# Optimization experiments

Hardware: AMD Instinct MI355X
Metric: run time of the kernel (lower is better)

Reference implementation:

```python
import jax, jax.numpy as jnp
import numpy as np

NUM_HEADS = 10
LN_EPS = 1e-5


def setup_inputs() -> dict:
    key = jax.random.key(0)
    ks = jax.random.split(key, 6)
    N, D = 4096, 640  # in_dim == out_dim required by residual add
    x = jax.random.normal(ks[0], (N, D), dtype=jnp.float32)
    s = 1.0 / np.sqrt(D)
    Wq = jax.random.normal(ks[1], (D, D), dtype=jnp.float32) * s  # torch Linear weight [out,in]
    Wk = jax.random.normal(ks[2], (D, D), dtype=jnp.float32) * s
    Wv = jax.random.normal(ks[3], (D, D), dtype=jnp.float32) * s
    gamma = jnp.ones((D,), dtype=jnp.float32)
    beta = jnp.zeros((D,), dtype=jnp.float32)
    return {"x": x, "Wq": Wq, "Wk": Wk, "Wv": Wv, "gamma": gamma, "beta": beta}


def reference(x, Wq, Wk, Wv, gamma, beta):
    N, D = x.shape
    dk = D // NUM_HEADS
    Q = x @ Wq.T  # [N, D]
    K = x @ Wk.T
    V = x @ Wv.T
    # Faithful to source: raw reshapes (NOT transposes)
    Qh = Q.reshape(NUM_HEADS, N, dk)
    Kh = K.reshape(NUM_HEADS, N, dk).reshape(NUM_HEADS, dk, N)  # torch.reshape, not .mT
    Vh = V.reshape(NUM_HEADS, N, dk)
    # Faithful quirk: scale by sqrt(K.shape[2]) == sqrt(N)
    scale = np.float32(np.sqrt(N))
    wghts = jax.nn.softmax((Qh @ Kh) / scale, axis=-1)  # [H, N, N]
    values = wghts @ Vh  # [H, N, dk]
    values = values.reshape(N, NUM_HEADS * dk)  # raw reshape merge
    values = values + x  # residual
    # LayerNorm(out_dim), biased variance, eps=1e-5
    mean = jnp.mean(values, axis=-1, keepdims=True)
    var = jnp.mean(jnp.square(values - mean), axis=-1, keepdims=True)
    out = (values - mean) * jax.lax.rsqrt(var + LN_EPS) * gamma + beta
    return out
```

## Files before the change

### kernel.cpp

```cpp
#include <hip/hip_runtime.h>
#if __has_include(<hip/hip_fp8.h>)
#include <hip/hip_fp8.h>
#endif


typedef __bf16 bf16x8 __attribute__((ext_vector_type(8)));
typedef __bf16 bf16x4 __attribute__((ext_vector_type(4)));
typedef float  f32x4  __attribute__((ext_vector_type(4)));
typedef unsigned short u16x4 __attribute__((ext_vector_type(4)));
typedef unsigned int   u32x4 __attribute__((ext_vector_type(4)));
typedef long           la64  __attribute__((may_alias));
typedef unsigned int   ua32  __attribute__((may_alias));

#define N_TOK   4096
#define D_MODEL 640
#define DK      64
#define HSLAB   (N_TOK * DK)
#define SQS 0.15014030f

#if __has_builtin(__builtin_amdgcn_exp2f)
#define EXP2(x) __builtin_amdgcn_exp2f(x)
#else
#define EXP2(x) exp2f(x)
#endif

__device__ __forceinline__ void stage16(const void* g, void* lds_uniform) {
    __builtin_amdgcn_global_load_lds(
        (const __attribute__((address_space(1))) unsigned int*)g,
        (__attribute__((address_space(3))) unsigned int*)lds_uniform, 16, 0, 0);
}

__device__ __forceinline__ u16x4 cvt4(f32x4 v) {
    return __builtin_bit_cast(u16x4, __builtin_convertvector(v, bf16x4));
}

__device__ __forceinline__ unsigned int pk_fp8(f32x4 v) {
#if __has_builtin(__builtin_amdgcn_cvt_pk_fp8_f32)
    int r = 0;
    r = __builtin_amdgcn_cvt_pk_fp8_f32(v[0], v[1], r, false);
    r = __builtin_amdgcn_cvt_pk_fp8_f32(v[2], v[3], r, true);
    return (unsigned int)r;
#else
    union { unsigned char b[4]; unsigned int u; } x;
    x.b[0] = __hip_fp8_e4m3(v[0]).__x;
    x.b[1] = __hip_fp8_e4m3(v[1]).__x;
    x.b[2] = __hip_fp8_e4m3(v[2]).__x;
    x.b[3] = __hip_fp8_e4m3(v[3]).__x;
    return x.u;
#endif
}

__global__ __launch_bounds__(256) void cvt_all(const float* __restrict__ x,
                                               const float* __restrict__ w0,
                                               const float* __restrict__ w1,
                                               const float* __restrict__ w2,
                                               unsigned short* __restrict__ xb,
                                               unsigned short* __restrict__ d0,
                                               unsigned short* __restrict__ d1,
                                               unsigned short* __restrict__ d2,
                                               f32x4* __restrict__ ltot4) {
    int i = blockIdx.x * 256 + threadIdx.x;
    if (i >= 962560) { ltot4[i - 962560] = (f32x4){0.f, 0.f, 0.f, 0.f}; return; }
    const float* s; unsigned short* d; int off; float scl = 1.0f;
    if (i < 655360) { s = x; d = xb; off = i; }
    else {
        int j = i - 655360;
        int w = j / 102400; off = j - w * 102400;
        s = (w == 0) ? w0 : (w == 1) ? w1 : w2;
        d = (w == 0) ? d0 : (w == 1) ? d1 : d2;
        if (w < 2) scl = SQS;
    }
    f32x4 v = ((const f32x4*)s)[off];
    v[0] *= scl; v[1] *= scl; v[2] *= scl; v[3] *= scl;
    ((u16x4*)d)[off] = cvt4(v);
}

__global__ __launch_bounds__(256, 2) void gemm_qkv(
    const unsigned short* __restrict__ xb,
    const unsigned short* __restrict__ wq,
    const unsigned short* __restrict__ wk,
    const unsigned short* __restrict__ wv,
    unsigned short* __restrict__ Qo,
    unsigned short* __restrict__ Ko,
    unsigned short* __restrict__ Vo) {
    const int b = blockIdx.x;
    const int g = b & 31;
    const int r = b >> 5;
    const int mode = r / 5;
    const int m0 = g * 128;
    const int n0 = (r % 5) * 128;
    const unsigned short* W = (mode == 0) ? wq : (mode == 1) ? wk : wv;
    unsigned short*       C = (mode == 0) ? Qo : (mode == 1) ? Ko : Vo;

    __shared__ unsigned short As[8192];
    __shared__ unsigned short Bs[8192];

    const int tid  = threadIdx.x;
    const int lane = tid & 63;
    const int wave = tid >> 6;
    const int quad = lane >> 4, l16 = lane & 15;
    const int wm = (wave >> 1) * 64, wn = (wave & 1) * 64;
    const int swz = l16 & 7;

    f32x4 acc[4][4] = {};

    int prow[4], pcol[4], lbase[4];
    for (int j = 0; j < 4; j++) {
        int p = j * 256 + tid;
        prow[j] = p >> 3;
        pcol[j] = ((p & 7) ^ (prow[j] & 7)) * 8;
        lbase[j] = (j * 256 + wave * 64) * 8;
    }

    for (int kt = 0; kt < D_MODEL; kt += 64) {
        __syncthreads();
        for (int j = 0; j < 4; j++) {
            stage16(&xb[(size_t)(m0 + prow[j]) * D_MODEL + kt + pcol[j]], As + lbase[j]);
            stage16(&W [(size_t)(n0 + prow[j]) * D_MODEL + kt + pcol[j]], Bs + lbase[j]);
        }
        __syncthreads();

        for (int s = 0; s < 2; s++) {
            bf16x8 af[4], bfr[4];
            for (int mi = 0; mi < 4; mi++) {
                int row = wm + mi * 16 + l16;
                af[mi] = *(const bf16x8*)&As[row * 64 + (((s << 2) + quad) ^ swz) * 8];
            }
            for (int ni = 0; ni < 4; ni++) {
                int row = wn + ni * 16 + l16;
                bfr[ni] = *(const bf16x8*)&Bs[row * 64 + (((s << 2) + quad) ^ swz) * 8];
            }
            for (int mi = 0; mi < 4; mi++)
                for (int ni = 0; ni < 4; ni++)
                    acc[mi][ni] = __builtin_amdgcn_mfma_f32_16x16x32_bf16(af[mi], bfr[ni], acc[mi][ni], 0, 0, 0);
        }
    }

    for (int mi = 0; mi < 4; mi++)
        for (int ni = 0; ni < 4; ni++) {
            u16x4 cv = cvt4(acc[mi][ni]);
            for (int r2 = 0; r2 < 4; r2++) {
                int row = m0 + wm + mi * 16 + quad * 4 + r2;
                int col = n0 + wn + ni * 16 + l16;
                C[(size_t)row * D_MODEL + col] = cv[r2];
            }
        }
}

__global__ __launch_bounds__(256) void transpose_kv(
    const unsigned short* __restrict__ Kn, unsigned char* __restrict__ Kp8,
    const unsigned short* __restrict__ Vn, unsigned char* __restrict__ Vp8,
    const unsigned short* __restrict__ Qn, unsigned char* __restrict__ Qf8) {
    const int z = blockIdx.z;
    const int t = threadIdx.x;

    if (z >= 20) {
        const size_t base = (size_t)(z - 20) * HSLAB + blockIdx.x * 4096 + t * 16;
        bf16x8 v0 = *(const bf16x8*)&Qn[base];
        bf16x8 v1 = *(const bf16x8*)&Qn[base + 8];
        f32x4 a = {(float)v0[0], (float)v0[1], (float)v0[2], (float)v0[3]};
        f32x4 b = {(float)v0[4], (float)v0[5], (float)v0[6], (float)v0[7]};
        f32x4 c = {(float)v1[0], (float)v1[1], (float)v1[2], (float)v1[3]};
        f32x4 d = {(float)v1[4], (float)v1[5], (float)v1[6], (float)v1[7]};
        u32x4 o = {pk_fp8(a), pk_fp8(b), pk_fp8(c), pk_fp8(d)};
        *(u32x4*)&Qf8[base] = o;
        return;
    }

    __shared__ unsigned short T[64][66];
    const unsigned short* src; unsigned char* dst;
    int R, Cc, r0, c0;
    if (z < 10) { src = Kn; dst = Kp8; R = 64;   Cc = 4096; r0 = 0; c0 = blockIdx.x * 64; }
    else        { src = Vn; dst = Vp8; R = 4096; Cc = 64;   r0 = blockIdx.x * 64; c0 = 0; }
    const size_t hb = (size_t)(z % 10) * HSLAB;
    const int rr = t >> 3, c8 = (t & 7) * 8;

    for (int hf = 0; hf < 2; hf++) {
        int r = rr + hf * 32;
        bf16x8 v = *(const bf16x8*)&src[hb + (size_t)(r0 + r) * Cc + c0 + c8];
        for (int j = 0; j < 8; j++) T[r][c8 + j] = ((unsigned short*)&v)[j];
    }
    __syncthreads();
    const bf16x8 zz = {};
    for (int hf = 0; hf < 2; hf++) {
        int r = rr + hf * 32;
        *(bf16x8*)&((unsigned short*)src)[hb + (size_t)(r0 + r) * Cc + c0 + c8] = zz;
    }
    for (int hf = 0; hf < 2; hf++) {
        int oc = rr + hf * 32;
        f32x4 lo, hi;
        for (int j = 0; j < 4; j++) {
            lo[j] = __builtin_bit_cast(float, (unsigned int)T[c8 + j][oc] << 16);
            hi[j] = __builtin_bit_cast(float, (unsigned int)T[c8 + 4 + j][oc] << 16);
        }
        uint2 ov; ov.x = pk_fp8(lo); ov.y = pk_fp8(hi);
        size_t dcol = (z < 10) ? ((size_t)(c0 + oc) * 64 + r0 + c8)
                               : ((size_t)oc * 4096 + r0 + c8);
        *(uint2*)&dst[hb + dcol] = ov;
    }
}

__global__ __launch_bounds__(256, 4) void attn(
    const unsigned char* __restrict__ Qf8,
    const unsigned char* __restrict__ Kp8,
    const unsigned char* __restrict__ Vp8,
    float* __restrict__ vals,
    float* __restrict__ l_tot) {
    const int h  = blockIdx.x >> 5;
    const int qt = blockIdx.x & 31;
    const int ntile = (blockIdx.y == 2) ? 10 : 11;
    const int tile0 = blockIdx.y * 11;
    const int lane = threadIdx.x & 63;
    const int wave = threadIdx.x >> 6;
    const int quad = lane >> 4, l16 = lane & 15;
    const size_t hoff = (size_t)h * HSLAB;

    __shared__ unsigned char sm[40960];
    unsigned char* const Kb0 = sm;
    unsigned char* const Kb1 = sm + 8192;
    unsigned char* const Vt  = sm + 16384;
    unsigned char* const Pw  = sm + 24576 + wave * 4096;

    const int qbase = qt * 128 + wave * 32;
    long qd[2][2];
    for (int g = 0; g < 2; g++) {
        const unsigned char* qp = Qf8 + hoff + (size_t)(qbase + g * 16 + l16) * 64 + quad * 8;
        qd[g][0] = *(const la64*)(qp);
        qd[g][1] = *(const la64*)(qp + 32);
    }

    f32x4 o[2][4] = {};
    f32x4 ol[2] = {};
    const long ONES8 = 0x3838383838383838L;

    const int cA = wave * 64 + lane, cB = cA + 256;
    const int kKeyA = ((cA >> 5) << 3) + (cA & 7), kCiA = (cA >> 3) & 3;
    const int kKeyB = ((cB >> 5) << 3) + (cB & 7), kCiB = (cB >> 3) & 3;
    const int vDkA  = ((cA >> 6) << 3) + (cA & 7), vCvA = (cA >> 3) & 7;
    const int vDkB  = ((cB >> 6) << 3) + (cB & 7), vCvB = (cB >> 3) & 7;

    const int kfb = (l16 >> 3) * 512 + (quad >> 1) * 128 + (l16 & 7) * 16 + (quad & 1) * 8;
    const int vfb = (l16 >> 3) * 1024 + (quad >> 1) * 128 + (l16 & 7) * 16 + (quad & 1) * 8;

    {
        const int keyb = tile0 << 7;
        stage16(Kp8 + hoff + (size_t)(keyb + kKeyA) * 64 + kCiA * 16, Kb0 + wave * 1024);
        stage16(Kp8 + hoff + (size_t)(keyb + kKeyB) * 64 + kCiB * 16, Kb0 + 4096 + wave * 1024);
    }

    for (int t = 0; t < ntile; t++) {
        const int keyb = (tile0 + t) << 7;
        unsigned char* const Kcur = (t & 1) ? Kb1 : Kb0;

        __syncthreads();

        if (t + 1 < ntile) {
            const int keyn = (tile0 + t + 1) << 7;
            unsigned char* const Knext = (t & 1) ? Kb0 : Kb1;
            stage16(Kp8 + hoff + (size_t)(keyn + kKeyA) * 64 + kCiA * 16, Knext + wave * 1024);
            stage16(Kp8 + hoff + (size_t)(keyn + kKeyB) * 64 + kCiB * 16, Knext + 4096 + wave * 1024);
        }
        stage16(Vp8 + hoff + (size_t)vDkA * N_TOK + keyb + vCvA * 16, Vt + wave * 1024);
        stage16(Vp8 + hoff + (size_t)vDkB * N_TOK + keyb + vCvB * 16, Vt + 4096 + wave * 1024);

        for (int ni = 0; ni < 8; ni++) {
            const unsigned char* kp = Kcur + ni * 1024 + kfb;
            long a0 = *(const la64*)(kp);
            long a1 = *(const la64*)(kp + 256);
            for (int g = 0; g < 2; g++) {
                f32x4 s = {};
                s = __builtin_amdgcn_mfma_f32_16x16x32_fp8_fp8(a0, qd[g][0], s, 0, 0, 0);
                s = __builtin_amdgcn_mfma_f32_16x16x32_fp8_fp8(a1, qd[g][1], s, 0, 0, 0);
                f32x4 pv;
                for (int r = 0; r < 4; r++) pv[r] = EXP2(s[r]);
                *(ua32*)(Pw + (ni * 2 + (quad >> 1)) * 256 +
                         (g * 16 + l16) * 8 + (quad & 1) * 4) = pk_fp8(pv);
            }
        }

        __syncthreads();

        for (int ks = 0; ks < 4; ks++) {
            long vf[4];
            for (int nd = 0; nd < 4; nd++)
                vf[nd] = *(const la64*)(Vt + nd * 2048 + ks * 256 + vfb);
            for (int g = 0; g < 2; g++) {
                long pf = *(const la64*)(Pw + (ks * 4 + quad) * 256 + (g * 16 + l16) * 8);
                ol[g] = __builtin_amdgcn_mfma_f32_16x16x32_fp8_fp8(pf, ONES8, ol[g], 0, 0, 0);
                for (int nd = 0; nd < 4; nd++)
                    o[g][nd] = __builtin_amdgcn_mfma_f32_16x16x32_fp8_fp8(pf, vf[nd], o[g][nd], 0, 0, 0);
            }
        }
    }

    if (l16 == 0)
        for (int g = 0; g < 2; g++)
            for (int r = 0; r < 4; r++)
                atomicAdd(&l_tot[(h << 12) + qbase + g * 16 + quad * 4 + r], ol[g][r]);

    for (int g = 0; g < 2; g++)
        for (int nd = 0; nd < 4; nd++)
            for (int r = 0; r < 4; r++) {
                int q = qbase + g * 16 + quad * 4 + r;
                atomicAdd(&vals[hoff + (size_t)q * DK + nd * 16 + l16], o[g][nd][r]);
            }
}

__global__ __launch_bounds__(256) void ln_kernel(
    const float* __restrict__ vals, const float* __restrict__ l_tot,
    const float* __restrict__ x,
    const float* __restrict__ gamma, const float* __restrict__ beta,
    float* __restrict__ out) {
    const int wave = threadIdx.x >> 6, lane = threadIdx.x & 63;
    const int row  = blockIdx.x * 4 + wave;
    const float* v  = vals + (size_t)row * D_MODEL;
    const float* xr = x    + (size_t)row * D_MODEL;

    float t[10];
    float s = 0.f;
    for (int i = 0; i < 10; i++) {
        float linv = 1.0f / l_tot[row * 10 + i];
        t[i] = v[lane + i * 64] * linv + xr[lane + i * 64];
        s += t[i];
    }
    for (int off = 32; off; off >>= 1) s += __shfl_xor(s, off, 64);
    float mean = s * (1.0f / 640.0f);
    float s2 = 0.f;
    for (int i = 0; i < 10; i++) { float d = t[i] - mean; s2 += d * d; }
    for (int off = 32; off; off >>= 1) s2 += __shfl_xor(s2, off, 64);
    float inv = rsqrtf(s2 * (1.0f / 640.0f) + 1e-5f);

    float* orow = out + (size_t)row * D_MODEL;
    for (int i = 0; i < 10; i++) {
        int c = lane + i * 64;
        orow[c] = (t[i] - mean) * inv * gamma[c] + beta[c];
    }
}

extern "C" void kernel_launch(void* const* d_in, const int* in_sizes, int n_in,
                              void* d_out, int out_size, void* d_ws, size_t ws_size,
                              hipStream_t stream) {
    const float* x     = (const float*)d_in[0];
    const float* Wq    = (const float*)d_in[1];
    const float* Wk    = (const float*)d_in[2];
    const float* Wv    = (const float*)d_in[3];
    const float* gamma = (const float*)d_in[4];
    const float* beta  = (const float*)d_in[5];
    float* out = (float*)d_out;

    char* ws = (char*)d_ws;
    unsigned short* xb  = (unsigned short*)(ws);
    unsigned char*  Qf8 = (unsigned char*)(ws);
    unsigned short* wqb = (unsigned short*)(ws + 5242880);
    unsigned short* wkb = (unsigned short*)(ws + 6062080);
    unsigned short* wvb = (unsigned short*)(ws + 6881280);
    unsigned short* Qn  = (unsigned short*)(ws + 7700480);
    unsigned char*  Kp8 = (unsigned char*)(ws + 12943360);
    unsigned char*  Vp8 = (unsigned char*)(ws + 18186240);
    unsigned short* Kn  = (unsigned short*)(ws + 23429120);
    unsigned short* Vn  = (unsigned short*)(ws + 28672000);
    float*          vals  = (float*)(ws + 23429120);
    float*          l_tot = (float*)(ws + 33914880);

    cvt_all<<<3800, 256, 0, stream>>>(x, Wq, Wk, Wv, xb, wqb, wkb, wvb,
                                      (f32x4*)l_tot);

    gemm_qkv<<<480, 256, 0, stream>>>(xb, wqb, wkb, wvb, Qn, Kn, Vn);

    transpose_kv<<<dim3(64, 1, 30), 256, 0, stream>>>(Kn, Kp8, Vn, Vp8, Qn, Qf8);

    attn<<<dim3(320, 3), 256, 0, stream>>>(Qf8, Kp8, Vp8, vals, l_tot);
    ln_kernel<<<1024, 256, 0, stream>>>(vals, l_tot, x, gamma, beta, out);
}
```

Before: 153.3 us.

## Fuse fp32-to-bf16 conversion into QKV GEMM and drop cvt_all kernel

Removes the separate cvt_all pre-pass. The QKV GEMM now stages fp32 x and weights directly into LDS, converts them to bf16 when loading fragments, and applies the 1/sqrt scale to the Q and K outputs in the epilogue. Zeroing of the l_tot accumulator moves into the transpose kernel. This saves one launch and a bf16 round trip through memory, but doubles LDS footprint (64KB per block) and global read bytes per tile inside the GEMM, and adds conversion work to the inner loop, which may hurt occupancy.

```diff
diff --git a/kernel.cpp b/kernel.cpp
--- a/kernel.cpp
+++ b/kernel.cpp
@@ -7,10 +7,12 @@
 typedef __bf16 bf16x8 __attribute__((ext_vector_type(8)));
 typedef __bf16 bf16x4 __attribute__((ext_vector_type(4)));
 typedef float  f32x4  __attribute__((ext_vector_type(4)));
+typedef float  f32x8  __attribute__((ext_vector_type(8)));
 typedef unsigned short u16x4 __attribute__((ext_vector_type(4)));
 typedef unsigned int   u32x4 __attribute__((ext_vector_type(4)));
 typedef long           la64  __attribute__((may_alias));
 typedef unsigned int   ua32  __attribute__((may_alias));
+typedef float          laf4  __attribute__((ext_vector_type(4), aligned(16))) ;
 
 #define N_TOK   4096
 #define D_MODEL 640
@@ -32,6 +34,13 @@
 
 __device__ __forceinline__ u16x4 cvt4(f32x4 v) {
     return __builtin_bit_cast(u16x4, __builtin_convertvector(v, bf16x4));
+}
+
+__device__ __forceinline__ bf16x8 pack8(f32x4 lo, f32x4 hi) {
+    f32x8 c;
+    c[0] = lo[0]; c[1] = lo[1]; c[2] = lo[2]; c[3] = lo[3];
+    c[4] = hi[0]; c[5] = hi[1]; c[6] = hi[2]; c[7] = hi[3];
+    return __builtin_convertvector(c, bf16x8);
 }
 
 __device__ __forceinline__ unsigned int pk_fp8(f32x4 v) {
@@ -50,36 +59,11 @@
 #endif
 }
 
-__global__ __launch_bounds__(256) void cvt_all(const float* __restrict__ x,
-                                               const float* __restrict__ w0,
-                                               const float* __restrict__ w1,
-                                               const float* __restrict__ w2,
-                                               unsigned short* __restrict__ xb,
-                                               unsigned short* __restrict__ d0,
-                                               unsigned short* __restrict__ d1,
-                                               unsigned short* __restrict__ d2,
-                                               f32x4* __restrict__ ltot4) {
-    int i = blockIdx.x * 256 + threadIdx.x;
-    if (i >= 962560) { ltot4[i - 962560] = (f32x4){0.f, 0.f, 0.f, 0.f}; return; }
-    const float* s; unsigned short* d; int off; float scl = 1.0f;
-    if (i < 655360) { s = x; d = xb; off = i; }
-    else {
-        int j = i - 655360;
-        int w = j / 102400; off = j - w * 102400;
-        s = (w == 0) ? w0 : (w == 1) ? w1 : w2;
-        d = (w == 0) ? d0 : (w == 1) ? d1 : d2;
-        if (w < 2) scl = SQS;
-    }
-    f32x4 v = ((const f32x4*)s)[off];
-    v[0] *= scl; v[1] *= scl; v[2] *= scl; v[3] *= scl;
-    ((u16x4*)d)[off] = cvt4(v);
-}
-
 __global__ __launch_bounds__(256, 2) void gemm_qkv(
-    const unsigned short* __restrict__ xb,
-    const unsigned short* __restrict__ wq,
-    const unsigned short* __restrict__ wk,
-    const unsigned short* __restrict__ wv,
+    const float* __restrict__ xf,
+    const float* __restrict__ wq,
+    const float* __restrict__ wk,
+    const float* __restrict__ wv,
     unsigned short* __restrict__ Qo,
     unsigned short* __restrict__ Ko,
     unsigned short* __restrict__ Vo) {
@@ -89,46 +73,56 @@
     const int mode = r / 5;
     const int m0 = g * 128;
     const int n0 = (r % 5) * 128;
-    const unsigned short* W = (mode == 0) ? wq : (mode == 1) ? wk : wv;
-    unsigned short*       C = (mode == 0) ? Qo : (mode == 1) ? Ko : Vo;
-
-    __shared__ unsigned short As[8192];
-    __shared__ unsigned short Bs[8192];
+    const float* W = (mode == 0) ? wq : (mode == 1) ? wk : wv;
+    unsigned short* C = (mode == 0) ? Qo : (mode == 1) ? Ko : Vo;
+    const float escale = (mode < 2) ? SQS : 1.0f;
+
+    __shared__ float As[8192];
+    __shared__ float Bs[8192];
 
     const int tid  = threadIdx.x;
     const int lane = tid & 63;
     const int wave = tid >> 6;
     const int quad = lane >> 4, l16 = lane & 15;
     const int wm = (wave >> 1) * 64, wn = (wave & 1) * 64;
-    const int swz = l16 & 7;
 
     f32x4 acc[4][4] = {};
 
-    int prow[4], pcol[4], lbase[4];
-    for (int j = 0; j < 4; j++) {
-        int p = j * 256 + tid;
-        prow[j] = p >> 3;
-        pcol[j] = ((p & 7) ^ (prow[j] & 7)) * 8;
-        lbase[j] = (j * 256 + wave * 64) * 8;
+    int prow[8], pcol[8];
+    for (int j = 0; j < 8; j++) {
+        int c = j * 256 + tid;
+        prow[j] = c >> 4;
+        pcol[j] = ((c & 15) ^ (prow[j] & 15)) * 4;
     }
 
     for (int kt = 0; kt < D_MODEL; kt += 64) {
         __syncthreads();
-        for (int j = 0; j < 4; j++) {
-            stage16(&xb[(size_t)(m0 + prow[j]) * D_MODEL + kt + pcol[j]], As + lbase[j]);
-            stage16(&W [(size_t)(n0 + prow[j]) * D_MODEL + kt + pcol[j]], Bs + lbase[j]);
+        for (int j = 0; j < 8; j++) {
+            char* dst = (char*)As + j * 4096 + wave * 1024;
+            stage16(&xf[(size_t)(m0 + prow[j]) * D_MODEL + kt + pcol[j]], dst);
+            char* dstB = (char*)Bs + j * 4096 + wave * 1024;
+            stage16(&W [(size_t)(n0 + prow[j]) * D_MODEL + kt + pcol[j]], dstB);
         }
         __syncthreads();
 
         for (int s = 0; s < 2; s++) {
+            const int u0 = s * 8 + quad * 2;
             bf16x8 af[4], bfr[4];
             for (int mi = 0; mi < 4; mi++) {
                 int row = wm + mi * 16 + l16;
-                af[mi] = *(const bf16x8*)&As[row * 64 + (((s << 2) + quad) ^ swz) * 8];
+                int r15 = row & 15;
+                const float* base = As + row * 64;
+                f32x4 lo = *(const laf4*)(base + ((u0     ^ r15) * 4));
+                f32x4 hi = *(const laf4*)(base + (((u0+1) ^ r15) * 4));
+                af[mi] = pack8(lo, hi);
             }
             for (int ni = 0; ni < 4; ni++) {
                 int row = wn + ni * 16 + l16;
-                bfr[ni] = *(const bf16x8*)&Bs[row * 64 + (((s << 2) + quad) ^ swz) * 8];
+                int r15 = row & 15;
+                const float* base = Bs + row * 64;
+                f32x4 lo = *(const laf4*)(base + ((u0     ^ r15) * 4));
+                f32x4 hi = *(const laf4*)(base + (((u0+1) ^ r15) * 4));
+                bfr[ni] = pack8(lo, hi);
             }
             for (int mi = 0; mi < 4; mi++)
                 for (int ni = 0; ni < 4; ni++)
@@ -138,7 +132,9 @@
 
     for (int mi = 0; mi < 4; mi++)
         for (int ni = 0; ni < 4; ni++) {
-            u16x4 cv = cvt4(acc[mi][ni]);
+            f32x4 a = acc[mi][ni];
+            a[0] *= escale; a[1] *= escale; a[2] *= escale; a[3] *= escale;
+            u16x4 cv = cvt4(a);
             for (int r2 = 0; r2 < 4; r2++) {
                 int row = m0 + wm + mi * 16 + quad * 4 + r2;
                 int col = n0 + wn + ni * 16 + l16;
@@ -150,12 +146,16 @@
 __global__ __launch_bounds__(256) void transpose_kv(
     const unsigned short* __restrict__ Kn, unsigned char* __restrict__ Kp8,
     const unsigned short* __restrict__ Vn, unsigned char* __restrict__ Vp8,
-    const unsigned short* __restrict__ Qn, unsigned char* __restrict__ Qf8) {
+    const unsigned short* __restrict__ Qn, unsigned char* __restrict__ Qf8,
+    f32x4* __restrict__ ltot4) {
     const int z = blockIdx.z;
     const int t = threadIdx.x;
 
     if (z >= 20) {
-        const size_t base = (size_t)(z - 20) * HSLAB + blockIdx.x * 4096 + t * 16;
+        const int hq = z - 20;
+        if (t < 16)
+            ltot4[hq * 1024 + blockIdx.x * 16 + t] = (f32x4){0.f, 0.f, 0.f, 0.f};
+        const size_t base = (size_t)hq * HSLAB + blockIdx.x * 4096 + t * 16;
         bf16x8 v0 = *(const bf16x8*)&Qn[base];
         bf16x8 v1 = *(const bf16x8*)&Qn[base + 8];
         f32x4 a = {(float)v0[0], (float)v0[1], (float)v0[2], (float)v0[3]};
@@ -349,11 +349,7 @@
     float* out = (float*)d_out;
 
     char* ws = (char*)d_ws;
-    unsigned short* xb  = (unsigned short*)(ws);
     unsigned char*  Qf8 = (unsigned char*)(ws);
-    unsigned short* wqb = (unsigned short*)(ws + 5242880);
-    unsigned short* wkb = (unsigned short*)(ws + 6062080);
-    unsigned short* wvb = (unsigned short*)(ws + 6881280);
     unsigned short* Qn  = (unsigned short*)(ws + 7700480);
     unsigned char*  Kp8 = (unsigned char*)(ws + 12943360);
     unsigned char*  Vp8 = (unsigned char*)(ws + 18186240);
@@ -362,12 +358,10 @@
     float*          vals  = (float*)(ws + 23429120);
     float*          l_tot = (float*)(ws + 33914880);
 
-    cvt_all<<<3800, 256, 0, stream>>>(x, Wq, Wk, Wv, xb, wqb, wkb, wvb,
-                                      (f32x4*)l_tot);
-
-    gemm_qkv<<<480, 256, 0, stream>>>(xb, wqb, wkb, wvb, Qn, Kn, Vn);
-
-    transpose_kv<<<dim3(64, 1, 30), 256, 0, stream>>>(Kn, Kp8, Vn, Vp8, Qn, Qf8);
+    gemm_qkv<<<480, 256, 0, stream>>>(x, Wq, Wk, Wv, Qn, Kn, Vn);
+
+    transpose_kv<<<dim3(64, 1, 30), 256, 0, stream>>>(Kn, Kp8, Vn, Vp8, Qn, Qf8,
+                                                      (f32x4*)l_tot);
 
     attn<<<dim3(320, 3), 256, 0, stream>>>(Qf8, Kp8, Vp8, vals, l_tot);
     ln_kernel<<<1024, 256, 0, stream>>>(vals, l_tot, x, gamma, beta, out);
```

New measurement: 155.8 us. No clear change (+1.6%).
